# Kernel optimization log

Hardware: AMD Instinct MI355X
Metric: run time of the kernel (lower is better)

Reference implementation:

```python
import jax, jax.numpy as jnp
import numpy as np

N_NODES = 32000
N_EDGES = 320000
N_GRAPHS = 1600
HID = 128
RBF = 32
ZDIM = 2 * HID + RBF  # CGConv concat dim = 288


def setup_inputs() -> dict:
    key = jax.random.key(0)
    ks = jax.random.split(key, 20)
    inp = {
        "x": jax.random.randint(ks[0], (N_NODES,), 0, 100),
        "edge_index": jax.random.randint(ks[1], (2, N_EDGES), 0, N_NODES),
        "edge_attr": jax.random.normal(ks[2], (N_EDGES, RBF), dtype=jnp.float32),
        "batch": jnp.sort(jax.random.randint(ks[3], (N_NODES,), 0, N_GRAPHS)),
        "emb": jax.random.normal(ks[4], (100, HID), dtype=jnp.float32) * 0.02,
    }
    s = 1.0 / np.sqrt(ZDIM)
    for i, k0 in zip((1, 2, 3), range(5, 11, 2)):
        inp[f"Wf{i}"] = jax.random.uniform(ks[k0], (ZDIM, HID), jnp.float32, -s, s)
        inp[f"bf{i}"] = jnp.zeros((HID,), jnp.float32)
        inp[f"Ws{i}"] = jax.random.uniform(ks[k0 + 1], (ZDIM, HID), jnp.float32, -s, s)
        inp[f"bs{i}"] = jnp.zeros((HID,), jnp.float32)
    sl = 1.0 / np.sqrt(HID)
    inp["Wlin"] = jax.random.uniform(ks[11], (HID, HID), jnp.float32, -sl, sl)
    inp["blin"] = jnp.zeros((HID,), jnp.float32)
    return inp


def _cgconv(h, src, dst, ea, Wf, bf, Ws, bs):
    # PyG CGConv: z = [x_i, x_j, e_ij]; msg = sigmoid(lin_f(z)) * softplus(lin_s(z)); out = x + sum_j msg
    z = jnp.concatenate([h[dst], h[src], ea], axis=1)  # [E, 288]
    msg = jax.nn.sigmoid(z @ Wf + bf) * jax.nn.softplus(z @ Ws + bs)  # [E, 128]
    return h + jax.ops.segment_sum(msg, dst, num_segments=N_NODES)


def reference(x, edge_index, edge_attr, batch, emb,
              Wf1, bf1, Ws1, bs1, Wf2, bf2, Ws2, bs2, Wf3, bf3, Ws3, bs3,
              Wlin, blin):
    src, dst = edge_index[0], edge_index[1]
    h = emb[x]  # [N, 128] embedding lookup
    h = jax.nn.relu(_cgconv(h, src, dst, edge_attr, Wf1, bf1, Ws1, bs1))
    h = jax.nn.relu(_cgconv(h, src, dst, edge_attr, Wf2, bf2, Ws2, bs2))
    h = jax.nn.relu(_cgconv(h, src, dst, edge_attr, Wf3, bf3, Ws3, bs3))
    # global mean pool over graphs
    sums = jax.ops.segment_sum(h, batch, num_segments=N_GRAPHS)  # [G, 128]
    cnt = jax.ops.segment_sum(jnp.ones((N_NODES,), h.dtype), batch, num_segments=N_GRAPHS)
    pooled = sums / jnp.maximum(cnt, 1.0)[:, None]
    return pooled @ Wlin + blin  # [G, 128]
```

## Files before the change

kernel.cpp:

```cpp
#include <hip/hip_runtime.h>
#include <math.h>

#define NN 32000
#define NE 320000
#define NG 1600

using frag_ab = __attribute__((ext_vector_type(8))) short;
using frag_cd = __attribute__((ext_vector_type(4))) float;

static __device__ __forceinline__ unsigned short f2bf(float f) {
  unsigned u = __builtin_bit_cast(unsigned, f);
  unsigned r = u + 0x7fff + ((u >> 16) & 1);
  return (unsigned short)(r >> 16);
}
static __device__ __forceinline__ float bflo(unsigned u) {
  return __builtin_bit_cast(float, u << 16);
}
static __device__ __forceinline__ float bfhi(unsigned u) {
  return __builtin_bit_cast(float, u & 0xffff0000u);
}

__global__ __launch_bounds__(256) void k_misc(const int* __restrict__ x,
                                              const float* __restrict__ emb,
                                              const float* __restrict__ Wf1, const float* __restrict__ Ws1,
                                              const float* __restrict__ Wf2, const float* __restrict__ Ws2,
                                              const float* __restrict__ Wf3, const float* __restrict__ Ws3,
                                              float* __restrict__ h,
                                              unsigned short* __restrict__ hb,
                                              unsigned short* __restrict__ accumb,
                                              unsigned short* __restrict__ wedge,
                                              unsigned short* __restrict__ wgemm) {
  int b = blockIdx.x;
  int tid = threadIdx.x;
  if (b < 2000) {
    int idx = b * 256 + tid;
    int n = idx >> 4;
    int c8 = (idx & 15) << 3;
    const float* e = emb + (size_t)x[n] * 128 + c8;
    float4 v0 = *(const float4*)e;
    float4 v1 = *(const float4*)(e + 4);
    float* hp = h + (size_t)n * 128 + c8;
    *(float4*)hp = v0;
    *(float4*)(hp + 4) = v1;
    ushort4 p0, p1;
    p0.x = f2bf(v0.x); p0.y = f2bf(v0.y); p0.z = f2bf(v0.z); p0.w = f2bf(v0.w);
    p1.x = f2bf(v1.x); p1.y = f2bf(v1.y); p1.z = f2bf(v1.z); p1.w = f2bf(v1.w);
    unsigned short* hbp = hb + (size_t)n * 128 + c8;
    *(ushort4*)hbp = p0;
    *(ushort4*)(hbp + 4) = p1;
    *(uint4*)(accumb + (size_t)n * 128 + c8) = make_uint4(0, 0, 0, 0);
  } else if (b < 2096) {
    int idx = (b - 2000) * 256 + tid;
    int l = idx >> 13;
    int r = idx & 8191;
    int cc = r >> 5;
    int k = r & 31;
    int w = cc >> 6, t = (cc >> 4) & 3, c = cc & 15;
    const float* Wf = (l == 0) ? Wf1 : (l == 1) ? Wf2 : Wf3;
    const float* Ws = (l == 0) ? Ws1 : (l == 1) ? Ws2 : Ws3;
    const float* W = (t < 2) ? Wf : Ws;
    int ch = w * 32 + 2 * c + (t & 1);
    wedge[(size_t)l * 8192 + cc * 32 + k] = f2bf(W[(size_t)(256 + k) * 128 + ch]);
  } else {
    int idx = (b - 2096) * 256 + tid;
    int l = idx >> 16;
    int r = idx & 65535;
    int cc = r >> 7;
    int k = r & 127;
    int seg = cc >> 7, within = cc & 127;
    int ch = (within & 96) + ((within & 15) << 1) + ((within >> 4) & 1);
    const float* Wf = (l == 0) ? Wf1 : (l == 1) ? Wf2 : Wf3;
    const float* Ws = (l == 0) ? Ws1 : (l == 1) ? Ws2 : Ws3;
    const float* W = (seg < 2) ? Wf : Ws;
    int krow = (seg & 1) * 128 + k;
    wgemm[(size_t)l * 65536 + cc * 128 + k] = f2bf(W[(size_t)krow * 128 + ch]);
  }
}

__global__ __launch_bounds__(256) void k_bstarts(const int* __restrict__ batch,
                                                 int* __restrict__ starts) {
  int n = blockIdx.x * 256 + threadIdx.x;
  if (n > NN) return;
  if (n == NN) {
    starts[NG] = NN;
    int last = batch[NN - 1];
    for (int g = last + 1; g < NG; ++g) starts[g] = NN;
  } else if (n == 0) {
    int b = batch[0];
    for (int g = 0; g <= b; ++g) starts[g] = 0;
  } else {
    int b0 = batch[n - 1], b1 = batch[n];
    for (int g = b0 + 1; g <= b1; ++g) starts[g] = n;
  }
}

__global__ __launch_bounds__(256) void k_hist(const int* __restrict__ ei,
                                              int* __restrict__ counts) {
  int e = blockIdx.x * 256 + threadIdx.x;
  atomicAdd(counts + ei[NE + e], 1);
}

__global__ __launch_bounds__(1024) void k_scan(const int* __restrict__ counts,
                                               int* __restrict__ offs) {
  __shared__ int part[1024];
  int t = threadIdx.x;
  int base = t * 32;
  int local[32];
  int sum = 0;
#pragma unroll
  for (int i = 0; i < 32; ++i) {
    int v = (base + i < NN) ? counts[base + i] : 0;
    local[i] = sum;
    sum += v;
  }
  part[t] = sum;
  __syncthreads();
  for (int off = 1; off < 1024; off <<= 1) {
    int v = (t >= off) ? part[t - off] : 0;
    __syncthreads();
    part[t] += v;
    __syncthreads();
  }
  int excl = (t == 0) ? 0 : part[t - 1];
#pragma unroll
  for (int i = 0; i < 32; ++i)
    if (base + i < NN) offs[base + i] = excl + local[i];
}

__global__ __launch_bounds__(256) void k_scatter(const int* __restrict__ ei,
                                                 const float* __restrict__ ea,
                                                 int* __restrict__ offs,
                                                 int* __restrict__ srcp,
                                                 int* __restrict__ dstp,
                                                 unsigned short* __restrict__ eab) {
  int e = blockIdx.x * 256 + threadIdx.x;
  int s = ei[e];
  int d = ei[NE + e];
  int pos = atomicAdd(offs + d, 1);
  srcp[pos] = s;
  dstp[pos] = d;
  int x = pos & 63;
  int p = (((x >> 2) & 3) << 4) | ((x >> 4) << 2) | (x & 3);
  unsigned short* q = eab + (size_t)((pos & ~63) | p) * 32;
  const float* a = ea + (size_t)e * 32;
#pragma unroll
  for (int i = 0; i < 4; ++i) {
    float4 v0 = *(const float4*)(a + i * 8);
    float4 v1 = *(const float4*)(a + i * 8 + 4);
    ushort4 o0, o1;
    o0.x = f2bf(v0.x); o0.y = f2bf(v0.y); o0.z = f2bf(v0.z); o0.w = f2bf(v0.w);
    o1.x = f2bf(v1.x); o1.y = f2bf(v1.y); o1.z = f2bf(v1.z); o1.w = f2bf(v1.w);
    *(ushort4*)(q + i * 8) = o0;
    *(ushort4*)(q + i * 8 + 4) = o1;
  }
}

__global__ __launch_bounds__(256) void k_gemm(const unsigned short* __restrict__ hb,
                                              const unsigned short* __restrict__ wgemmL,
                                              unsigned short* __restrict__ T) {
  __shared__ short sA[64 * 136];
  __shared__ short sB[128 * 136];
  int m0 = blockIdx.x * 64;
  int n0 = blockIdx.y * 128;
  int tid = threadIdx.x;
#pragma unroll
  for (int i = 0; i < 4; ++i) {
    int idx = tid + i * 256;
    int row = idx >> 4, chk = idx & 15;
    uint4 v = *(const uint4*)(hb + (size_t)(m0 + row) * 128 + chk * 8);
    *(uint4*)&sA[row * 136 + chk * 8] = v;
  }
#pragma unroll
  for (int i = 0; i < 8; ++i) {
    int idx = tid + i * 256;
    int col = idx >> 4, chk = idx & 15;
    uint4 v = *(const uint4*)(wgemmL + (size_t)(n0 + col) * 128 + chk * 8);
    *(uint4*)&sB[col * 136 + chk * 8] = v;
  }
  __syncthreads();
  int w = tid >> 6, lane = tid & 63, c = lane & 15, q = lane >> 4;
  frag_cd acc[4][2];
#pragma unroll
  for (int mt = 0; mt < 4; ++mt)
#pragma unroll
    for (int t = 0; t < 2; ++t) acc[mt][t] = (frag_cd){0.f, 0.f, 0.f, 0.f};
#pragma unroll
  for (int ks = 0; ks < 4; ++ks) {
    frag_ab Af[4], Bf[2];
#pragma unroll
    for (int mt = 0; mt < 4; ++mt)
      Af[mt] = *(const frag_ab*)&sA[(mt * 16 + c) * 136 + ks * 32 + q * 8];
#pragma unroll
    for (int t = 0; t < 2; ++t)
      Bf[t] = *(const frag_ab*)&sB[(w * 32 + t * 16 + c) * 136 + ks * 32 + q * 8];
#pragma unroll
    for (int mt = 0; mt < 4; ++mt)
#pragma unroll
      for (int t = 0; t < 2; ++t)
        acc[mt][t] = __builtin_amdgcn_mfma_f32_16x16x32_bf16(Af[mt], Bf[t], acc[mt][t], 0, 0, 0);
  }
  int nbase = n0 + w * 32 + 2 * c;
#pragma unroll
  for (int mt = 0; mt < 4; ++mt) {
#pragma unroll
    for (int r = 0; r < 4; ++r) {
      int node = m0 + mt * 16 + q * 4 + r;
      unsigned pk = (unsigned)f2bf(acc[mt][0][r]) | ((unsigned)f2bf(acc[mt][1][r]) << 16);
      *(unsigned*)(T + (size_t)node * 512 + nbase) = pk;
    }
  }
}

__global__ __launch_bounds__(256) void k_edge(const int* __restrict__ srcp,
                                              const int* __restrict__ dstp,
                                              const unsigned short* __restrict__ eab,
                                              const unsigned short* __restrict__ T,
                                              const unsigned short* __restrict__ wedgeL,
                                              const float* __restrict__ bf,
                                              const float* __restrict__ bs,
                                              unsigned short* __restrict__ accumb) {
  __shared__ short sA[64 * 40];
  __shared__ short sB[256 * 40];
  __shared__ float sbf[128], sbs[128];
  __shared__ int sSrc[64], sDst[64];
  int tid = threadIdx.x;
  int e0 = blockIdx.x * 64;
  {
    int row = tid >> 2, qq = tid & 3;
    uint4 v = *(const uint4*)(eab + (size_t)e0 * 32 + tid * 8);
    *(uint4*)&sA[row * 40 + qq * 8] = v;
  }
#pragma unroll
  for (int i = 0; i < 4; ++i) {
    int idx = tid + i * 256;
    int col = idx >> 2, qq = idx & 3;
    uint4 v = *(const uint4*)(wedgeL + (size_t)col * 32 + qq * 8);
    *(uint4*)&sB[col * 40 + qq * 8] = v;
  }
  if (tid < 128) {
    sbf[tid] = bf[tid];
    sbs[tid] = bs[tid];
  } else if (tid < 192) {
    sSrc[tid - 128] = srcp[e0 + tid - 128];
  } else {
    sDst[tid - 192] = dstp[e0 + tid - 192];
  }
  __syncthreads();

  int w = tid >> 6;
  int lane = tid & 63;
  int c = lane & 15;
  int q = lane >> 4;

  frag_ab Af[4], Bf[4];
#pragma unroll
  for (int et = 0; et < 4; ++et)
    Af[et] = *(const frag_ab*)&sA[(et * 16 + c) * 40 + q * 8];
#pragma unroll
  for (int t = 0; t < 4; ++t)
    Bf[t] = *(const frag_ab*)&sB[(w * 64 + t * 16 + c) * 40 + q * 8];

  frag_cd acc[4][4];
#pragma unroll
  for (int et = 0; et < 4; ++et)
#pragma unroll
    for (int t = 0; t < 4; ++t)
      acc[et][t] = (frag_cd){0.f, 0.f, 0.f, 0.f};
#pragma unroll
  for (int et = 0; et < 4; ++et)
#pragma unroll
    for (int t = 0; t < 4; ++t)
      acc[et][t] = __builtin_amdgcn_mfma_f32_16x16x32_bf16(Af[et], Bf[t], acc[et][t], 0, 0, 0);

  int ch = w * 32 + 2 * c;
  float bf0 = sbf[ch], bf1 = sbf[ch + 1];
  float bs0 = sbs[ch], bs1 = sbs[ch + 1];

  int prevd = sDst[q * 16];
  float a0 = 0.f, a1 = 0.f;
#pragma unroll
  for (int grp = 0; grp < 2; ++grp) {
    unsigned fsv[8], ssv[8], fdv[8], sdv[8];
#pragma unroll
    for (int i = 0; i < 8; ++i) {
      int e = q * 16 + grp * 8 + i;
      int s = sSrc[e], d = sDst[e];
      const unsigned short* Ts = T + (size_t)s * 512;
      const unsigned short* Td = T + (size_t)d * 512;
      fsv[i] = *(const unsigned*)(Ts + 128 + ch);
      ssv[i] = *(const unsigned*)(Ts + 384 + ch);
      fdv[i] = *(const unsigned*)(Td + ch);
      sdv[i] = *(const unsigned*)(Td + 256 + ch);
    }
    float m0[8], m1[8];
#pragma unroll
    for (int i = 0; i < 8; ++i) {
      int idx = grp * 8 + i;
      int et = idx >> 2, r = idx & 3;
      float xf0 = acc[et][0][r] + bflo(fdv[i]) + bflo(fsv[i]) + bf0;
      float xf1 = acc[et][1][r] + bfhi(fdv[i]) + bfhi(fsv[i]) + bf1;
      float xs0 = acc[et][2][r] + bflo(sdv[i]) + bflo(ssv[i]) + bs0;
      float xs1 = acc[et][3][r] + bfhi(sdv[i]) + bfhi(ssv[i]) + bs1;
      float g0 = __builtin_amdgcn_rcpf(1.f + __expf(-xf0));
      float g1 = __builtin_amdgcn_rcpf(1.f + __expf(-xf1));
      float sp0 = fmaxf(xs0, 0.f) + __logf(1.f + __expf(-fabsf(xs0)));
      float sp1 = fmaxf(xs1, 0.f) + __logf(1.f + __expf(-fabsf(xs1)));
      m0[i] = g0 * sp0;
      m1[i] = g1 * sp1;
    }
#pragma unroll
    for (int i = 0; i < 8; ++i) {
      int d = sDst[q * 16 + grp * 8 + i];
      if (d != prevd) {
        unsigned pk = (unsigned)f2bf(a0) | ((unsigned)f2bf(a1) << 16);
        unsigned short* p = accumb + (size_t)prevd * 128 + ch;
        asm volatile("global_atomic_pk_add_bf16 %0, %1, off" :: "v"(p), "v"(pk) : "memory");
        a0 = 0.f; a1 = 0.f;
        prevd = d;
      }
      a0 += m0[i];
      a1 += m1[i];
    }
  }
  {
    unsigned pk = (unsigned)f2bf(a0) | ((unsigned)f2bf(a1) << 16);
    unsigned short* p = accumb + (size_t)prevd * 128 + ch;
    asm volatile("global_atomic_pk_add_bf16 %0, %1, off" :: "v"(p), "v"(pk) : "memory");
  }
}

__global__ __launch_bounds__(256) void k_update(float* __restrict__ h,
                                                unsigned short* __restrict__ hb,
                                                unsigned short* __restrict__ accumb) {
  int idx = blockIdx.x * 256 + threadIdx.x;
  size_t off = (size_t)idx * 8;
  uint4 a = *(uint4*)(accumb + off);
  float4 v0 = *(float4*)(h + off);
  float4 v1 = *(float4*)(h + off + 4);
  v0.x = fmaxf(v0.x + bflo(a.x), 0.f);
  v0.y = fmaxf(v0.y + bfhi(a.x), 0.f);
  v0.z = fmaxf(v0.z + bflo(a.y), 0.f);
  v0.w = fmaxf(v0.w + bfhi(a.y), 0.f);
  v1.x = fmaxf(v1.x + bflo(a.z), 0.f);
  v1.y = fmaxf(v1.y + bfhi(a.z), 0.f);
  v1.z = fmaxf(v1.z + bflo(a.w), 0.f);
  v1.w = fmaxf(v1.w + bfhi(a.w), 0.f);
  *(float4*)(h + off) = v0;
  *(float4*)(h + off + 4) = v1;
  ushort4 p0, p1;
  p0.x = f2bf(v0.x); p0.y = f2bf(v0.y); p0.z = f2bf(v0.z); p0.w = f2bf(v0.w);
  p1.x = f2bf(v1.x); p1.y = f2bf(v1.y); p1.z = f2bf(v1.z); p1.w = f2bf(v1.w);
  *(ushort4*)(hb + off) = p0;
  *(ushort4*)(hb + off + 4) = p1;
  *(uint4*)(accumb + off) = make_uint4(0, 0, 0, 0);
}

__global__ __launch_bounds__(256) void k_update3(float* __restrict__ h,
                                                 const unsigned short* __restrict__ accumb) {
  int idx = blockIdx.x * 256 + threadIdx.x;
  size_t off = (size_t)idx * 8;
  uint4 a = *(uint4*)(accumb + off);
  float4 v0 = *(float4*)(h + off);
  float4 v1 = *(float4*)(h + off + 4);
  v0.x = fmaxf(v0.x + bflo(a.x), 0.f);
  v0.y = fmaxf(v0.y + bfhi(a.x), 0.f);
  v0.z = fmaxf(v0.z + bflo(a.y), 0.f);
  v0.w = fmaxf(v0.w + bfhi(a.y), 0.f);
  v1.x = fmaxf(v1.x + bflo(a.z), 0.f);
  v1.y = fmaxf(v1.y + bfhi(a.z), 0.f);
  v1.z = fmaxf(v1.z + bflo(a.w), 0.f);
  v1.w = fmaxf(v1.w + bfhi(a.w), 0.f);
  *(float4*)(h + off) = v0;
  *(float4*)(h + off + 4) = v1;
}

__global__ __launch_bounds__(128) void k_pool_final(const float* __restrict__ h,
                                                    const int* __restrict__ starts,
                                                    const float* __restrict__ Wlin,
                                                    const float* __restrict__ blin,
                                                    float* __restrict__ out) {
  __shared__ float p[128];
  int g = blockIdx.x, c = threadIdx.x;
  int s0 = starts[g], s1 = starts[g + 1];
  float acc = 0.f;
  for (int n = s0; n < s1; ++n) acc += h[(size_t)n * 128 + c];
  float inv = 1.f / fmaxf((float)(s1 - s0), 1.f);
  p[c] = acc * inv;
  __syncthreads();
  float o = blin[c];
#pragma unroll 8
  for (int k = 0; k < 128; ++k) o += p[k] * Wlin[k * 128 + c];
  out[(size_t)g * 128 + c] = o;
}

extern "C" void kernel_launch(void* const* d_in, const int* in_sizes, int n_in,
                              void* d_out, int out_size, void* d_ws, size_t ws_size,
                              hipStream_t stream) {
  const int* x = (const int*)d_in[0];
  const int* ei = (const int*)d_in[1];
  const float* ea = (const float*)d_in[2];
  const int* batch = (const int*)d_in[3];
  const float* emb = (const float*)d_in[4];
  const float* Wf[3] = {(const float*)d_in[5], (const float*)d_in[9], (const float*)d_in[13]};
  const float* bf[3] = {(const float*)d_in[6], (const float*)d_in[10], (const float*)d_in[14]};
  const float* Wsm[3] = {(const float*)d_in[7], (const float*)d_in[11], (const float*)d_in[15]};
  const float* bs[3] = {(const float*)d_in[8], (const float*)d_in[12], (const float*)d_in[16]};
  const float* Wlin = (const float*)d_in[17];
  const float* blin = (const float*)d_in[18];
  float* out = (float*)d_out;

  char* ws = (char*)d_ws;
  float* h = (float*)ws;                        ws += (size_t)NN * 128 * 4;
  unsigned short* hb = (unsigned short*)ws;     ws += (size_t)NN * 128 * 2;
  unsigned short* accumb = (unsigned short*)ws; ws += (size_t)NN * 128 * 2;
  unsigned short* T = (unsigned short*)ws;      ws += (size_t)NN * 512 * 2;
  unsigned short* eab = (unsigned short*)ws;    ws += (size_t)NE * 32 * 2;
  unsigned short* wedge = (unsigned short*)ws;  ws += 3 * 8192 * 2;
  unsigned short* wgemm = (unsigned short*)ws;  ws += 3 * 65536 * 2;
  int* counts = (int*)ws;                       ws += (size_t)NN * 4;
  int* offs = (int*)ws;                         ws += (size_t)NN * 4;
  int* srcp = (int*)ws;                         ws += (size_t)NE * 4;
  int* dstp = (int*)ws;                         ws += (size_t)NE * 4;
  int* starts = (int*)ws;                       ws += (size_t)(NG + 1) * 4;

  hipMemsetAsync(counts, 0, (size_t)NN * 4, stream);
  k_misc<<<2864, 256, 0, stream>>>(x, emb, Wf[0], Wsm[0], Wf[1], Wsm[1], Wf[2], Wsm[2],
                                   h, hb, accumb, wedge, wgemm);
  k_bstarts<<<126, 256, 0, stream>>>(batch, starts);
  k_hist<<<1250, 256, 0, stream>>>(ei, counts);
  k_scan<<<1, 1024, 0, stream>>>(counts, offs);
  k_scatter<<<1250, 256, 0, stream>>>(ei, ea, offs, srcp, dstp, eab);
  for (int l = 0; l < 3; ++l) {
    k_gemm<<<dim3(500, 4), 256, 0, stream>>>(hb, wgemm + (size_t)l * 65536, T);
    k_edge<<<5000, 256, 0, stream>>>(srcp, dstp, eab, T, wedge + (size_t)l * 8192,
                                     bf[l], bs[l], accumb);
    if (l < 2)
      k_update<<<2000, 256, 0, stream>>>(h, hb, accumb);
    else
      k_update3<<<2000, 256, 0, stream>>>(h, accumb);
  }
  k_pool_final<<<1600, 128, 0, stream>>>(h, starts, Wlin, blin, out);
}
```

Before: 427.9 us.

## Interleave per-node projection table so edge gathers use 8-byte loads

Reorders the columns of the node projection GEMM weights so each node's table row stores the f and s gate projections for a channel pair next to each other, dst half first and src half second. The edge kernel then does two 8-byte gathers per edge instead of four 4-byte gathers, and it precomputes row offsets when staging src/dst indices in shared memory. The elementwise math is written with 2-wide float vectors so the compiler can emit packed FP32 ops. This is meant to cut gather instruction count and address arithmetic in the memory-bound edge stage; it relies on the node GEMM output layout matching the new weight permutation.

```diff
diff --git a/kernel.cpp b/kernel.cpp
--- a/kernel.cpp
+++ b/kernel.cpp
@@ -7,6 +7,7 @@
 
 using frag_ab = __attribute__((ext_vector_type(8))) short;
 using frag_cd = __attribute__((ext_vector_type(4))) float;
+typedef float v2f __attribute__((ext_vector_type(2)));
 
 static __device__ __forceinline__ unsigned short f2bf(float f) {
   unsigned u = __builtin_bit_cast(unsigned, f);
@@ -18,6 +19,9 @@
 }
 static __device__ __forceinline__ float bfhi(unsigned u) {
   return __builtin_bit_cast(float, u & 0xffff0000u);
+}
+static __device__ __forceinline__ v2f unpk(unsigned u) {
+  return (v2f){bflo(u), bfhi(u)};
 }
 
 __global__ __launch_bounds__(256) void k_misc(const int* __restrict__ x,
@@ -67,12 +71,14 @@
     int r = idx & 65535;
     int cc = r >> 7;
     int k = r & 127;
-    int seg = cc >> 7, within = cc & 127;
-    int ch = (within & 96) + ((within & 15) << 1) + ((within >> 4) & 1);
+    int p = (cc & ~31) + ((cc & 15) << 1) + ((cc >> 4) & 1);
+    int ph = p & 255;
+    int j = ph >> 2, sub = ph & 3;
     const float* Wf = (l == 0) ? Wf1 : (l == 1) ? Wf2 : Wf3;
     const float* Ws = (l == 0) ? Ws1 : (l == 1) ? Ws2 : Ws3;
-    const float* W = (seg < 2) ? Wf : Ws;
-    int krow = (seg & 1) * 128 + k;
+    const float* W = (sub < 2) ? Wf : Ws;
+    int ch = 2 * j + (sub & 1);
+    int krow = ((p < 256) ? 0 : 128) + k;
     wgemm[(size_t)l * 65536 + cc * 128 + k] = f2bf(W[(size_t)krow * 128 + ch]);
   }
 }
@@ -241,9 +247,9 @@
     sbf[tid] = bf[tid];
     sbs[tid] = bs[tid];
   } else if (tid < 192) {
-    sSrc[tid - 128] = srcp[e0 + tid - 128];
+    sSrc[tid - 128] = srcp[e0 + tid - 128] * 512 + 256;
   } else {
-    sDst[tid - 192] = dstp[e0 + tid - 192];
+    sDst[tid - 192] = dstp[e0 + tid - 192] * 512;
   }
   __syncthreads();
 
@@ -273,58 +279,50 @@
       acc[et][t] = __builtin_amdgcn_mfma_f32_16x16x32_bf16(Af[et], Bf[t], acc[et][t], 0, 0, 0);
 
   int ch = w * 32 + 2 * c;
-  float bf0 = sbf[ch], bf1 = sbf[ch + 1];
-  float bs0 = sbs[ch], bs1 = sbs[ch + 1];
+  int jo = ch * 2;
+  v2f bfv = {sbf[ch], sbf[ch + 1]};
+  v2f bsv = {sbs[ch], sbs[ch + 1]};
 
   int prevd = sDst[q * 16];
-  float a0 = 0.f, a1 = 0.f;
+  v2f av = {0.f, 0.f};
 #pragma unroll
   for (int grp = 0; grp < 2; ++grp) {
-    unsigned fsv[8], ssv[8], fdv[8], sdv[8];
+    uint2 dv[8], sv[8];
 #pragma unroll
     for (int i = 0; i < 8; ++i) {
       int e = q * 16 + grp * 8 + i;
-      int s = sSrc[e], d = sDst[e];
-      const unsigned short* Ts = T + (size_t)s * 512;
-      const unsigned short* Td = T + (size_t)d * 512;
-      fsv[i] = *(const unsigned*)(Ts + 128 + ch);
-      ssv[i] = *(const unsigned*)(Ts + 384 + ch);
-      fdv[i] = *(const unsigned*)(Td + ch);
-      sdv[i] = *(const unsigned*)(Td + 256 + ch);
+      dv[i] = *(const uint2*)(T + sDst[e] + jo);
+      sv[i] = *(const uint2*)(T + sSrc[e] + jo);
     }
-    float m0[8], m1[8];
+    v2f m[8];
 #pragma unroll
     for (int i = 0; i < 8; ++i) {
       int idx = grp * 8 + i;
       int et = idx >> 2, r = idx & 3;
-      float xf0 = acc[et][0][r] + bflo(fdv[i]) + bflo(fsv[i]) + bf0;
-      float xf1 = acc[et][1][r] + bfhi(fdv[i]) + bfhi(fsv[i]) + bf1;
-      float xs0 = acc[et][2][r] + bflo(sdv[i]) + bflo(ssv[i]) + bs0;
-      float xs1 = acc[et][3][r] + bfhi(sdv[i]) + bfhi(ssv[i]) + bs1;
-      float g0 = __builtin_amdgcn_rcpf(1.f + __expf(-xf0));
-      float g1 = __builtin_amdgcn_rcpf(1.f + __expf(-xf1));
-      float sp0 = fmaxf(xs0, 0.f) + __logf(1.f + __expf(-fabsf(xs0)));
-      float sp1 = fmaxf(xs1, 0.f) + __logf(1.f + __expf(-fabsf(xs1)));
-      m0[i] = g0 * sp0;
-      m1[i] = g1 * sp1;
+      v2f xf = (v2f){acc[et][0][r], acc[et][1][r]} + unpk(dv[i].x) + unpk(sv[i].x) + bfv;
+      v2f xs = (v2f){acc[et][2][r], acc[et][3][r]} + unpk(dv[i].y) + unpk(sv[i].y) + bsv;
+      float g0 = __builtin_amdgcn_rcpf(1.f + __expf(-xf.x));
+      float g1 = __builtin_amdgcn_rcpf(1.f + __expf(-xf.y));
+      float sp0 = fmaxf(xs.x, 0.f) + __logf(1.f + __expf(-fabsf(xs.x)));
+      float sp1 = fmaxf(xs.y, 0.f) + __logf(1.f + __expf(-fabsf(xs.y)));
+      m[i] = (v2f){g0 * sp0, g1 * sp1};
     }
 #pragma unroll
     for (int i = 0; i < 8; ++i) {
       int d = sDst[q * 16 + grp * 8 + i];
       if (d != prevd) {
-        unsigned pk = (unsigned)f2bf(a0) | ((unsigned)f2bf(a1) << 16);
-        unsigned short* p = accumb + (size_t)prevd * 128 + ch;
+        unsigned pk = (unsigned)f2bf(av.x) | ((unsigned)f2bf(av.y) << 16);
+        unsigned short* p = accumb + (size_t)(prevd >> 2) + ch;
         asm volatile("global_atomic_pk_add_bf16 %0, %1, off" :: "v"(p), "v"(pk) : "memory");
-        a0 = 0.f; a1 = 0.f;
+        av = (v2f){0.f, 0.f};
         prevd = d;
       }
-      a0 += m0[i];
-      a1 += m1[i];
+      av += m[i];
     }
   }
   {
-    unsigned pk = (unsigned)f2bf(a0) | ((unsigned)f2bf(a1) << 16);
-    unsigned short* p = accumb + (size_t)prevd * 128 + ch;
+    unsigned pk = (unsigned)f2bf(av.x) | ((unsigned)f2bf(av.y) << 16);
+    unsigned short* p = accumb + (size_t)(prevd >> 2) + ch;
     asm volatile("global_atomic_pk_add_bf16 %0, %1, off" :: "v"(p), "v"(pk) : "memory");
   }
 }
```

Result: no change. 435.0 us (+1.6%).
